# Kernel optimization log

Measured on AMD Instinct MI355X. Metric: run time of the kernel, lower is better.

The kernel has to match this reference:

```python
import jax, jax.numpy as jnp
import numpy as np

DIM = 1024
N_HEAD = 16
SEQ = 2048
GATE_IN = 12
ROPE_BASE = 10000.0
ATTN_SCALE = 0.1
EPS = 1e-6


def setup_inputs() -> dict:
    key = jax.random.key(0)
    ks = jax.random.split(key, 8)
    std = 0.5 * DIM ** -0.5
    bound = (3.0 ** 0.5) * std
    x = jax.random.normal(ks[0], (1, SEQ, DIM), dtype=jnp.float32)
    v1 = jax.random.normal(ks[1], (1, SEQ, DIM), dtype=jnp.float32)
    Wq = jax.random.uniform(ks[2], (DIM, DIM), jnp.float32, -bound, bound)
    Wk = jax.random.uniform(ks[3], (DIM, DIM), jnp.float32, -bound, bound)
    Wv = jax.random.uniform(ks[4], (DIM, DIM), jnp.float32, -bound, bound)
    # original zero-inits c_proj/attn_gate; use small random so output is non-trivial
    Wproj = jax.random.normal(ks[5], (DIM, DIM), dtype=jnp.float32) * 0.02
    Wgate = jax.random.normal(ks[6], (N_HEAD, GATE_IN), dtype=jnp.float32) * 0.02
    lamb = jnp.float32(0.5)
    return {"x": x, "v1": v1, "Wq": Wq, "Wk": Wk, "Wv": Wv,
            "Wproj": Wproj, "lamb": lamb, "Wgate": Wgate}


def _rms_norm(t):
    return t * jax.lax.rsqrt(jnp.mean(jnp.square(t), axis=-1, keepdims=True) + EPS)


def _rotary(t):
    # t: [B, T, H, hd]; rotates halves per the module's sign convention
    B, T, H, hd = t.shape
    d = hd // 2
    inv_freq = 1.0 / (ROPE_BASE ** (jnp.arange(0, hd, 2, dtype=jnp.float32) / hd))  # [d]
    freqs = jnp.arange(T, dtype=jnp.float32)[:, None] * inv_freq[None, :]  # [T, d]
    cos = jnp.cos(freqs)[None, :, None, :]
    sin = jnp.sin(freqs)[None, :, None, :]
    x1, x2 = t[..., :d], t[..., d:]
    y1 = x1 * cos + x2 * sin
    y2 = -x1 * sin + x2 * cos
    return jnp.concatenate([y1, y2], axis=-1)


def reference(x, v1, Wq, Wk, Wv, Wproj, lamb, Wgate):
    B, T, dim = x.shape
    H = Wgate.shape[0]
    hd = dim // H

    q = (x @ Wq.T).reshape(B, T, H, hd)
    k = (x @ Wk.T).reshape(B, T, H, hd)
    v = (x @ Wv.T).reshape(B, T, H, hd)

    # lambda-blended value mixing with residual value stream v1
    v = (1.0 - lamb) * v + lamb * v1.reshape(B, T, H, hd)

    q, k = _rms_norm(q), _rms_norm(k)
    q, k = _rotary(q), _rotary(k)

    # causal attention with fixed scale 0.1 (flex_attention block-sparse causal)
    scores = jnp.einsum("bthd,bshd->bhts", q, k) * ATTN_SCALE  # [B,H,T,T]
    causal = jnp.tril(jnp.ones((T, T), dtype=bool))
    scores = jnp.where(causal[None, None], scores, jnp.float32(-1e30))
    probs = jax.nn.softmax(scores, axis=-1)
    y = jnp.einsum("bhts,bshd->bthd", probs, v)  # [B,T,H,hd]

    # sigmoid gate from the first 12 channels of x, per head
    gate = jax.nn.sigmoid(x[..., :Wgate.shape[1]] @ Wgate.T)[..., None]  # [B,T,H,1]
    y = (y * gate).reshape(B, T, dim)
    y = y @ Wproj.T
    return y, v1
```

## Files before the change

### kernel.cpp

```cpp
#include <hip/hip_runtime.h>
#include <hip/hip_bf16.h>

#define T_SEQ 2048
#define NH 16
#define HD 64
#define SCALE_LOG2E 0.14426950408889634f

typedef __attribute__((ext_vector_type(8))) short bf16x8;
typedef __attribute__((ext_vector_type(4))) short bf16x4;
typedef __attribute__((ext_vector_type(4))) float f32x4;

__device__ __forceinline__ short f2bs(float f) {
  union { float f; unsigned u; } v; v.f = f;
  unsigned r = v.u + 0x7fffu + ((v.u >> 16) & 1u);
  return (short)(r >> 16);
}

__device__ __forceinline__ float bs2f(short s) {
  union { unsigned u; float f; } v;
  v.u = ((unsigned)(unsigned short)s) << 16;
  return v.f;
}

__device__ __forceinline__ unsigned cvt_pk_bf16(float lo, float hi) {
  unsigned r;
  asm("v_cvt_pk_bf16_f32 %0, %1, %2" : "=v"(r) : "v"(lo), "v"(hi));
  return r;
}

__device__ __forceinline__ void gload16(const short* g, short* l) {
  __builtin_amdgcn_global_load_lds(
      (const __attribute__((address_space(1))) void*)g,
      (__attribute__((address_space(3))) void*)l, 16, 0, 0);
}

__global__ __launch_bounds__(256) void prep(const float* __restrict__ x,
                                            const float* __restrict__ wq,
                                            const float* __restrict__ wk,
                                            const float* __restrict__ wv,
                                            const float* __restrict__ wp,
                                            const float* __restrict__ v1,
                                            const float* __restrict__ Wg,
                                            short* __restrict__ xbT,
                                            short* __restrict__ wqkvT,
                                            short* __restrict__ wpjT,
                                            float* __restrict__ out2,
                                            float* __restrict__ gate,
                                            float2* __restrict__ rope) {
  const int rt = blockIdx.x;
  const int tid = threadIdx.x;
  if (blockIdx.y == 8) {
    int id = rt * 256 + tid;
    int t = id >> 4, h = id & 15;
    float acc = 0.f;
    #pragma unroll
    for (int i = 0; i < 12; ++i) acc += x[(size_t)t * 1024 + i] * Wg[h * 12 + i];
    gate[id] = 1.f / (1.f + __expf(-acc));
    #pragma unroll
    for (int j = 0; j < 2; ++j) {
      int e = id * 2 + j;
      int tt = e >> 5, p = e & 31;
      float invf = __builtin_exp2f(-0.41524101186092f * (float)p);
      float s, c;
      sincosf((float)tt * invf, &s, &c);
      rope[e] = make_float2(c, s);
    }
    return;
  }
  if (rt >= 96) {
    const int r0 = (rt - 96) * 64;
    const float* s = v1 + (size_t)r0 * 1024 + blockIdx.y * 128;
    float* d = out2 + (size_t)r0 * 1024 + blockIdx.y * 128;
    #pragma unroll
    for (int it = 0; it < 8; ++it) {
      int e = it * 256 + tid;
      int r = e >> 5, c4 = e & 31;
      *(float4*)&d[(size_t)r * 1024 + c4 * 4] = *(const float4*)&s[(size_t)r * 1024 + c4 * 4];
    }
    return;
  }
  __shared__ __attribute__((aligned(16))) short lv[64][136];
  const float* src; short* dst; int srow0, drow0, R;
  if (rt < 32)      { src = x;  dst = xbT;   R = 2048; srow0 = rt * 64;        drow0 = srow0; }
  else if (rt < 48) { src = wq; dst = wqkvT; R = 3072; srow0 = (rt - 32) * 64; drow0 = srow0; }
  else if (rt < 64) { src = wk; dst = wqkvT; R = 3072; srow0 = (rt - 48) * 64; drow0 = srow0 + 1024; }
  else if (rt < 80) { src = wv; dst = wqkvT; R = 3072; srow0 = (rt - 64) * 64; drow0 = srow0 + 2048; }
  else              { src = wp; dst = wpjT;  R = 1024; srow0 = (rt - 80) * 64; drow0 = srow0; }
  const int c0 = blockIdx.y * 16;
  #pragma unroll
  for (int it = 0; it < 8; ++it) {
    int e = it * 256 + tid;
    int r = e >> 5, c4 = e & 31;
    float4 v = *(const float4*)&src[(size_t)(srow0 + r) * 1024 + blockIdx.y * 128 + c4 * 4];
    bf16x4 o; o[0] = f2bs(v.x); o[1] = f2bs(v.y); o[2] = f2bs(v.z); o[3] = f2bs(v.w);
    *(bf16x4*)&lv[r][c4 * 4] = o;
  }
  __syncthreads();
  #pragma unroll
  for (int it = 0; it < 4; ++it) {
    int e = it * 256 + tid;
    int kc = e >> 6, r = e & 63;
    bf16x8 w = *(const bf16x8*)&lv[r][kc * 8];
    *(bf16x8*)&dst[((size_t)(c0 + kc) * R + drow0 + r) * 8] = w;
  }
}

template <int BM, int BN, bool QKV>
__global__ __launch_bounds__(256) void gemm(const short* __restrict__ A,
                                            const short* __restrict__ B,
                                            float* __restrict__ C,
                                            short* __restrict__ qb,
                                            short* __restrict__ kb,
                                            short* __restrict__ vt,
                                            const float* __restrict__ v1,
                                            const float* __restrict__ lambp,
                                            const float2* __restrict__ rope,
                                            int M, int N, int K) {
  constexpr int MF = BM / 32, NB = BN / 32;
  constexpr int LA = BM / 64, LB = BN / 64;
  __shared__ union {
    struct { short As[3][4][BM][8]; short Bs[3][4][BN][8]; } g;
    short lv[BM][130];
  } sm;
  const int tid = threadIdx.x;
  const int lane = tid & 63, wid = tid >> 6;
  const int lr = lane & 15, lg = lane >> 4;
  const int wm = (wid >> 1) * (BM / 2), wn = (wid & 1) * (BN / 2);
  const int nper = gridDim.x >> 3;
  const int tile = (blockIdx.x & 7) * nper + (blockIdx.x >> 3);
  const int gx = M / BM;
  const int bm = (tile % gx) * BM, bn = (tile / gx) * BN;
  const short* Ap = A + ((size_t)wid * M + bm + lane) * 8;
  const short* Bp = B + ((size_t)wid * N + bn + lane) * 8;
  f32x4 acc[MF][NB] = {};
  auto stage = [&](int buf, int k0) {
    #pragma unroll
    for (int g = 0; g < LA; ++g)
      gload16(Ap + (size_t)k0 * M + g * 512, &sm.g.As[buf][wid][64 * g][0]);
    #pragma unroll
    for (int g = 0; g < LB; ++g)
      gload16(Bp + (size_t)k0 * N + g * 512, &sm.g.Bs[buf][wid][64 * g][0]);
  };
  auto compute = [&](int buf) {
    bf16x8 af[MF], bfr[NB];
    #pragma unroll
    for (int m = 0; m < MF; ++m) af[m] = *(const bf16x8*)&sm.g.As[buf][lg][wm + m * 16 + lr][0];
    #pragma unroll
    for (int n = 0; n < NB; ++n) bfr[n] = *(const bf16x8*)&sm.g.Bs[buf][lg][wn + n * 16 + lr][0];
    #pragma unroll
    for (int m = 0; m < MF; ++m)
      #pragma unroll
      for (int n = 0; n < NB; ++n)
        acc[m][n] = __builtin_amdgcn_mfma_f32_16x16x32_bf16(af[m], bfr[n], acc[m][n], 0, 0, 0);
  };
  const int nsteps = K >> 5;
  stage(0, 0);
  stage(1, 32);
  int cur = 0;
  for (int ks = 0; ks < nsteps - 1; ++ks) {
    if constexpr (LA + LB == 4)      asm volatile("s_waitcnt vmcnt(4)" ::: "memory");
    else if constexpr (LA + LB == 3) asm volatile("s_waitcnt vmcnt(3)" ::: "memory");
    else                             asm volatile("s_waitcnt vmcnt(2)" ::: "memory");
    __builtin_amdgcn_s_barrier();
    __builtin_amdgcn_sched_barrier(0);
    int s2 = cur + 2; if (s2 >= 3) s2 -= 3;
    if (ks + 2 < nsteps) stage(s2, (ks + 2) * 32);
    compute(cur);
    cur = (cur == 2) ? 0 : cur + 1;
  }
  asm volatile("s_waitcnt vmcnt(0)" ::: "memory");
  __builtin_amdgcn_s_barrier();
  __builtin_amdgcn_sched_barrier(0);
  compute(cur);

  if constexpr (QKV) {
    if (bn < 2048) {
      const bool isq = (bn < 1024);
      short* dst = isq ? qb : kb;
      const int h = ((bn + wn) & 1023) >> 6;
      #pragma unroll
      for (int m = 0; m < MF; ++m)
        #pragma unroll
        for (int r = 0; r < 4; ++r) {
          const int t = bm + wm + m * 16 + 4 * lg + r;
          float ss = acc[m][0][r] * acc[m][0][r] + acc[m][1][r] * acc[m][1][r]
                   + acc[m][2][r] * acc[m][2][r] + acc[m][3][r] * acc[m][3][r];
          ss += __shfl_xor(ss, 1);
          ss += __shfl_xor(ss, 2);
          ss += __shfl_xor(ss, 4);
          ss += __shfl_xor(ss, 8);
          const float rms = rsqrtf(ss * (1.f / 64.f) + 1e-6f);
          short* row = dst + ((size_t)h * T_SEQ + t) * 64;
          #pragma unroll
          for (int n2 = 0; n2 < 2; ++n2) {
            float x1 = acc[m][n2][r] * rms, x2 = acc[m][n2 + 2][r] * rms;
            float2 cs = rope[t * 32 + n2 * 16 + lr];
            float y1 = x1 * cs.x + x2 * cs.y;
            float y2 = x2 * cs.x - x1 * cs.y;
            if (isq) { y1 *= SCALE_LOG2E; y2 *= SCALE_LOG2E; }
            row[n2 * 16 + lr] = f2bs(y1);
            row[32 + n2 * 16 + lr] = f2bs(y2);
          }
        }
    } else {
      const float Lb = *lambp;
      const int h0 = (bn - 2048) >> 6;
      __syncthreads();
      #pragma unroll
      for (int m = 0; m < MF; ++m)
        #pragma unroll
        for (int r = 0; r < 4; ++r) {
          const int tl = wm + m * 16 + 4 * lg + r;
          const size_t vrow = (size_t)(bm + tl) * 1024 + h0 * 64;
          #pragma unroll
          for (int n = 0; n < NB; ++n) {
            const int col = wn + n * 16 + lr;
            float w = v1[vrow + col];
            sm.lv[tl][col] = f2bs((1.f - Lb) * acc[m][n][r] + Lb * w);
          }
        }
      __syncthreads();
      constexpr int TPB = BM / 8;
      #pragma unroll
      for (int it = 0; it < BM / 16; ++it) {
        int u = it * 256 + tid;
        int c0 = (u % TPB) * 8;
        int d = (u / TPB) & 63;
        int hh = u / (TPB * 64);
        bf16x8 w;
        #pragma unroll
        for (int j = 0; j < 8; ++j) {
          int c = c0 + j;
          int src = (c & 96) | ((c & 1) << 4) | ((c >> 1) & 15);
          w[j] = sm.lv[src][hh * 64 + d];
        }
        *(bf16x8*)&vt[((size_t)(h0 + hh) * 64 + d) * T_SEQ + bm + c0] = w;
      }
    }
  } else {
    #pragma unroll
    for (int m = 0; m < MF; ++m)
      #pragma unroll
      for (int r = 0; r < 4; ++r) {
        const int t = bm + wm + m * 16 + 4 * lg + r;
        float* Cr = C + (size_t)t * N + bn + wn + lr;
        #pragma unroll
        for (int n = 0; n < NB; ++n) Cr[n * 16] = acc[m][n][r];
      }
  }
}

__global__ __launch_bounds__(256) void attn(const short* __restrict__ qb,
                                            const short* __restrict__ kb,
                                            const short* __restrict__ vtp,
                                            short* __restrict__ partO,
                                            float* __restrict__ partL) {
  __shared__ __attribute__((aligned(16))) short Ks[2][4096];
  __shared__ __attribute__((aligned(16))) short Vs[2][4096];
  __shared__ __attribute__((aligned(16))) short p_lds[4][16][72];
  const int head = blockIdx.x & 15;
  const int b = blockIdx.x >> 4;
  int strip, qg;
  if (b < 32)      { strip = 0; qg = 31 - b; }
  else if (b < 56) { strip = 1; qg = 63 - b; }
  else if (b < 72) { strip = 2; qg = 87 - b; }
  else             { strip = 3; qg = 103 - b; }
  const int nt = min(8, qg + 1 - strip * 8);
  const int lane = threadIdx.x & 63, wid = threadIdx.x >> 6;
  const int lr = lane & 15, lg = lane >> 4;
  const int qt0 = qg * 64 + wid * 16;
  const short* Q = qb + (size_t)head * (T_SEQ * HD);
  const short* Kp = kb + (size_t)head * (T_SEQ * HD);
  const short* Vt = vtp + (size_t)head * (HD * T_SEQ);
  short (*P)[72] = p_lds[wid];

  bf16x8 aq0 = *(const bf16x8*)&Q[(size_t)(qt0 + lr) * HD + 8 * lg];
  bf16x8 aq1 = *(const bf16x8*)&Q[(size_t)(qt0 + lr) * HD + 32 + 8 * lg];
  f32x4 accO[4] = {};
  float lsum[4] = {0.f, 0.f, 0.f, 0.f};

  auto stage = [&](int buf, int jg) {
    const int kv0 = jg * 64;
    #pragma unroll
    for (int i = 0; i < 2; ++i) {
      int s = i * 256 + wid * 64 + lane;
      int row = s >> 3;
      int cG = (s & 7) ^ (row & 7);
      gload16(Kp + (size_t)(kv0 + row) * HD + cG * 8,
              &Ks[buf][(size_t)(i * 256 + wid * 64) * 8]);
      gload16(Vt + (size_t)row * T_SEQ + kv0 + cG * 8,
              &Vs[buf][(size_t)(i * 256 + wid * 64) * 8]);
    }
  };
  stage(0, strip * 8);
  for (int j = 0; j < nt; ++j) {
    const int jg = strip * 8 + j;
    __syncthreads();
    if (j + 1 < nt) stage((j + 1) & 1, jg + 1);
    const short* Kb = Ks[j & 1];
    const short* Vb = Vs[j & 1];
    f32x4 st[4];
    #pragma unroll
    for (int t = 0; t < 4; ++t) {
      int row = 16 * t + lr;
      int c0 = lg ^ (row & 7);
      bf16x8 k0 = *(const bf16x8*)&Kb[row * 64 + c0 * 8];
      bf16x8 k1 = *(const bf16x8*)&Kb[row * 64 + (c0 ^ 4) * 8];
      f32x4 s = {};
      s = __builtin_amdgcn_mfma_f32_16x16x32_bf16(aq0, k0, s, 0, 0, 0);
      s = __builtin_amdgcn_mfma_f32_16x16x32_bf16(aq1, k1, s, 0, 0, 0);
      st[t] = s;
    }
    if (jg == qg) {
      #pragma unroll
      for (int t = 0; t < 4; ++t)
        #pragma unroll
        for (int r = 0; r < 4; ++r)
          st[t][r] = (16 * t + lr > wid * 16 + 4 * lg + r) ? -1e30f : st[t][r];
    }
    #pragma unroll
    for (int r = 0; r < 4; ++r) {
      float p0 = __builtin_exp2f(st[0][r]);
      float p1 = __builtin_exp2f(st[1][r]);
      float p2 = __builtin_exp2f(st[2][r]);
      float p3 = __builtin_exp2f(st[3][r]);
      lsum[r] += (p0 + p1) + (p2 + p3);
      *(unsigned*)&P[4 * lg + r][2 * lr] = cvt_pk_bf16(p0, p1);
      *(unsigned*)&P[4 * lg + r][32 + 2 * lr] = cvt_pk_bf16(p2, p3);
    }
    asm volatile("s_waitcnt lgkmcnt(0)" ::: "memory");
    __builtin_amdgcn_sched_barrier(0);
    bf16x8 pa0 = *(const bf16x8*)&P[lr][8 * lg];
    bf16x8 pa1 = *(const bf16x8*)&P[lr][32 + 8 * lg];
    #pragma unroll
    for (int nv = 0; nv < 4; ++nv) {
      int row0 = nv * 16 + lr;
      int c0 = lg ^ (row0 & 7);
      bf16x8 v0 = *(const bf16x8*)&Vb[row0 * 64 + c0 * 8];
      bf16x8 v1e = *(const bf16x8*)&Vb[row0 * 64 + (c0 ^ 4) * 8];
      accO[nv] = __builtin_amdgcn_mfma_f32_16x16x32_bf16(pa0, v0, accO[nv], 0, 0, 0);
      accO[nv] = __builtin_amdgcn_mfma_f32_16x16x32_bf16(pa1, v1e, accO[nv], 0, 0, 0);
    }
  }
  short* pO = partO + (size_t)(head * 80 + b) * 4096;
  float* pL = partL + (size_t)(head * 80 + b) * 64;
  #pragma unroll
  for (int r = 0; r < 4; ++r) {
    float sres = lsum[r];
    sres += __shfl_xor(sres, 1);
    sres += __shfl_xor(sres, 2);
    sres += __shfl_xor(sres, 4);
    sres += __shfl_xor(sres, 8);
    int row = wid * 16 + 4 * lg + r;
    #pragma unroll
    for (int nv = 0; nv < 4; ++nv)
      pO[row * 64 + nv * 16 + lr] = f2bs(accO[nv][r]);
    if (lr == 0) pL[row] = sres;
  }
}

__global__ __launch_bounds__(256) void attn_reduce(const short* __restrict__ partO,
                                                   const float* __restrict__ partL,
                                                   const float* __restrict__ gate,
                                                   short* __restrict__ obT) {
  const int head = blockIdx.x & 15;
  const int qg = blockIdx.x >> 4;
  const int ns = (qg >> 3) + 1;
  const int tid = threadIdx.x;
  const int row = tid >> 2, q4 = tid & 3;
  const int sbase[4] = {0, 32, 56, 72};
  f32x4 o[4] = {};
  float l = 0.f;
  for (int s = 0; s < ns; ++s) {
    const int slot = head * 80 + sbase[s] + 31 - qg;
    const short* pb = partO + (size_t)slot * 4096;
    #pragma unroll
    for (int c = 0; c < 4; ++c) {
      bf16x4 v = *(const bf16x4*)&pb[row * 64 + q4 * 16 + c * 4];
      #pragma unroll
      for (int j = 0; j < 4; ++j) o[c][j] += bs2f(v[j]);
    }
    l += partL[(size_t)slot * 64 + row];
  }
  const int t = qg * 64 + row;
  const float gs = gate[t * 16 + head] / l;
  const int cg0 = head * 8 + q4 * 2;
  bf16x8 w0, w1;
  #pragma unroll
  for (int j = 0; j < 4; ++j) {
    w0[j]     = f2bs(o[0][j] * gs);
    w0[4 + j] = f2bs(o[1][j] * gs);
    w1[j]     = f2bs(o[2][j] * gs);
    w1[4 + j] = f2bs(o[3][j] * gs);
  }
  *(bf16x8*)&obT[((size_t)cg0 * 2048 + t) * 8] = w0;
  *(bf16x8*)&obT[((size_t)(cg0 + 1) * 2048 + t) * 8] = w1;
}

extern "C" void kernel_launch(void* const* d_in, const int* in_sizes, int n_in,
                              void* d_out, int out_size, void* d_ws, size_t ws_size,
                              hipStream_t stream) {
  const float* x     = (const float*)d_in[0];
  const float* v1    = (const float*)d_in[1];
  const float* Wq    = (const float*)d_in[2];
  const float* Wk    = (const float*)d_in[3];
  const float* Wv    = (const float*)d_in[4];
  const float* Wproj = (const float*)d_in[5];
  const float* lamb  = (const float*)d_in[6];
  const float* Wgate = (const float*)d_in[7];
  float* out = (float*)d_out;

  char* ws = (char*)d_ws;
  short*  xbT   = (short*)(ws);
  short*  wqkvT = (short*)(ws + ((size_t)4  << 20));
  short*  wpjT  = (short*)(ws + ((size_t)10 << 20));
  short*  partO = (short*)(ws + ((size_t)12 << 20));
  float*  partL = (float*)(ws + ((size_t)23 << 20));
  float2* rope  = (float2*)(ws + ((size_t)34 << 20));
  short*  qb    = (short*)(ws + ((size_t)36 << 20));
  short*  kb    = (short*)(ws + ((size_t)40 << 20));
  short*  vt    = (short*)(ws + ((size_t)44 << 20));
  float*  gate  = (float*)(ws + ((size_t)48 << 20));
  short*  obT   = xbT;

  prep<<<dim3(128, 9), 256, 0, stream>>>(x, Wq, Wk, Wv, Wproj, v1, Wgate,
                                         xbT, wqkvT, wpjT,
                                         out + (size_t)T_SEQ * 1024, gate, rope);
  gemm<64, 128, true><<<768, 256, 0, stream>>>(xbT, wqkvT, nullptr, qb, kb, vt,
                                               v1, lamb, rope, 2048, 3072, 1024);
  attn<<<1280, 256, 0, stream>>>(qb, kb, vt, partO, partL);
  attn_reduce<<<512, 256, 0, stream>>>(partO, partL, gate, obT);
  gemm<64, 64, false><<<512, 256, 0, stream>>>(obT, wpjT, out, nullptr, nullptr,
                                               nullptr, nullptr, nullptr, nullptr,
                                               2048, 1024, 1024);
}
```

Measured before the change: 73.31 us.

## Fuse attention reduce into attn via atomic last-block, move v1 copy to proj gemm

```diff
diff --git a/kernel.cpp b/kernel.cpp
--- a/kernel.cpp
+++ b/kernel.cpp
@@ -39,18 +39,18 @@
                                             const float* __restrict__ wk,
                                             const float* __restrict__ wv,
                                             const float* __restrict__ wp,
-                                            const float* __restrict__ v1,
                                             const float* __restrict__ Wg,
                                             short* __restrict__ xbT,
                                             short* __restrict__ wqkvT,
                                             short* __restrict__ wpjT,
-                                            float* __restrict__ out2,
                                             float* __restrict__ gate,
-                                            float2* __restrict__ rope) {
+                                            float2* __restrict__ rope,
+                                            int* __restrict__ cnt) {
   const int rt = blockIdx.x;
   const int tid = threadIdx.x;
   if (blockIdx.y == 8) {
     int id = rt * 256 + tid;
+    if (id < 512) cnt[id] = 0;
     int t = id >> 4, h = id & 15;
     float acc = 0.f;
     #pragma unroll
@@ -67,18 +67,7 @@
     }
     return;
   }
-  if (rt >= 96) {
-    const int r0 = (rt - 96) * 64;
-    const float* s = v1 + (size_t)r0 * 1024 + blockIdx.y * 128;
-    float* d = out2 + (size_t)r0 * 1024 + blockIdx.y * 128;
-    #pragma unroll
-    for (int it = 0; it < 8; ++it) {
-      int e = it * 256 + tid;
-      int r = e >> 5, c4 = e & 31;
-      *(float4*)&d[(size_t)r * 1024 + c4 * 4] = *(const float4*)&s[(size_t)r * 1024 + c4 * 4];
-    }
-    return;
-  }
+  if (rt >= 96) return;
   __shared__ __attribute__((aligned(16))) short lv[64][136];
   const float* src; short* dst; int srow0, drow0, R;
   if (rt < 32)      { src = x;  dst = xbT;   R = 2048; srow0 = rt * 64;        drow0 = srow0; }
@@ -115,9 +104,22 @@
                                             const float* __restrict__ v1,
                                             const float* __restrict__ lambp,
                                             const float2* __restrict__ rope,
-                                            int M, int N, int K) {
+                                            int M, int N, int K, int ngemm) {
   constexpr int MF = BM / 32, NB = BN / 32;
   constexpr int LA = BM / 64, LB = BN / 64;
+  if constexpr (!QKV) {
+    if ((int)blockIdx.x >= ngemm) {
+      const int cb = blockIdx.x - ngemm;
+      const float* s = v1 + (size_t)cb * 8192;
+      float* d = C + (size_t)T_SEQ * 1024 + (size_t)cb * 8192;
+      #pragma unroll
+      for (int it = 0; it < 8; ++it) {
+        int e = it * 256 + threadIdx.x;
+        *(float4*)&d[e * 4] = *(const float4*)&s[e * 4];
+      }
+      return;
+    }
+  }
   __shared__ union {
     struct { short As[3][4][BM][8]; short Bs[3][4][BN][8]; } g;
     short lv[BM][130];
@@ -126,7 +128,7 @@
   const int lane = tid & 63, wid = tid >> 6;
   const int lr = lane & 15, lg = lane >> 4;
   const int wm = (wid >> 1) * (BM / 2), wn = (wid & 1) * (BN / 2);
-  const int nper = gridDim.x >> 3;
+  const int nper = ngemm >> 3;
   const int tile = (blockIdx.x & 7) * nper + (blockIdx.x >> 3);
   const int gx = M / BM;
   const int bm = (tile % gx) * BM, bn = (tile / gx) * BN;
@@ -254,10 +256,14 @@
                                             const short* __restrict__ kb,
                                             const short* __restrict__ vtp,
                                             short* __restrict__ partO,
-                                            float* __restrict__ partL) {
+                                            float* __restrict__ partL,
+                                            const float* __restrict__ gate,
+                                            short* __restrict__ obT,
+                                            int* __restrict__ cnt) {
   __shared__ __attribute__((aligned(16))) short Ks[2][4096];
   __shared__ __attribute__((aligned(16))) short Vs[2][4096];
   __shared__ __attribute__((aligned(16))) short p_lds[4][16][72];
+  __shared__ int last_flag;
   const int head = blockIdx.x & 15;
   const int b = blockIdx.x >> 4;
   int strip, qg;
@@ -266,7 +272,8 @@
   else if (b < 72) { strip = 2; qg = 87 - b; }
   else             { strip = 3; qg = 103 - b; }
   const int nt = min(8, qg + 1 - strip * 8);
-  const int lane = threadIdx.x & 63, wid = threadIdx.x >> 6;
+  const int tid = threadIdx.x;
+  const int lane = tid & 63, wid = tid >> 6;
   const int lr = lane & 15, lg = lane >> 4;
   const int qt0 = qg * 64 + wid * 16;
   const short* Q = qb + (size_t)head * (T_SEQ * HD);
@@ -357,16 +364,16 @@
       pO[row * 64 + nv * 16 + lr] = f2bs(accO[nv][r]);
     if (lr == 0) pL[row] = sres;
   }
-}
-
-__global__ __launch_bounds__(256) void attn_reduce(const short* __restrict__ partO,
-                                                   const float* __restrict__ partL,
-                                                   const float* __restrict__ gate,
-                                                   short* __restrict__ obT) {
-  const int head = blockIdx.x & 15;
-  const int qg = blockIdx.x >> 4;
+
   const int ns = (qg >> 3) + 1;
-  const int tid = threadIdx.x;
+  __threadfence();
+  if (tid == 0) {
+    int old = atomicAdd(&cnt[head * 32 + qg], 1);
+    last_flag = (old == ns - 1);
+  }
+  __syncthreads();
+  if (!last_flag) return;
+  __threadfence();
   const int row = tid >> 2, q4 = tid & 3;
   const int sbase[4] = {0, 32, 56, 72};
   f32x4 o[4] = {};
@@ -416,6 +423,7 @@
   short*  wpjT  = (short*)(ws + ((size_t)10 << 20));
   short*  partO = (short*)(ws + ((size_t)12 << 20));
   float*  partL = (float*)(ws + ((size_t)23 << 20));
+  int*    cnt   = (int*)  (ws + ((size_t)33 << 20));
   float2* rope  = (float2*)(ws + ((size_t)34 << 20));
   short*  qb    = (short*)(ws + ((size_t)36 << 20));
   short*  kb    = (short*)(ws + ((size_t)40 << 20));
@@ -423,14 +431,12 @@
   float*  gate  = (float*)(ws + ((size_t)48 << 20));
   short*  obT   = xbT;
 
-  prep<<<dim3(128, 9), 256, 0, stream>>>(x, Wq, Wk, Wv, Wproj, v1, Wgate,
-                                         xbT, wqkvT, wpjT,
-                                         out + (size_t)T_SEQ * 1024, gate, rope);
+  prep<<<dim3(128, 9), 256, 0, stream>>>(x, Wq, Wk, Wv, Wproj, Wgate,
+                                         xbT, wqkvT, wpjT, gate, rope, cnt);
   gemm<64, 128, true><<<768, 256, 0, stream>>>(xbT, wqkvT, nullptr, qb, kb, vt,
-                                               v1, lamb, rope, 2048, 3072, 1024);
-  attn<<<1280, 256, 0, stream>>>(qb, kb, vt, partO, partL);
-  attn_reduce<<<512, 256, 0, stream>>>(partO, partL, gate, obT);
-  gemm<64, 64, false><<<512, 256, 0, stream>>>(obT, wpjT, out, nullptr, nullptr,
-                                               nullptr, nullptr, nullptr, nullptr,
-                                               2048, 1024, 1024);
-}
+                                               v1, lamb, rope, 2048, 3072, 1024, 768);
+  attn<<<1280, 256, 0, stream>>>(qb, kb, vt, partO, partL, gate, obT, cnt);
+  gemm<64, 64, false><<<768, 256, 0, stream>>>(obT, wpjT, out, nullptr, nullptr,
+                                               nullptr, v1, nullptr, nullptr,
+                                               2048, 1024, 1024, 512);
+}
```

After: 278.5 us. +280.0%, slower.
